# Kernel optimization log

Measured on AMD Instinct MI355X. Metric: run time of the kernel, lower is better.

## Reference

```python
import jax, jax.numpy as jnp
import numpy as np

E, K = 8, 2            # num_experts, top_k
H, DFF = 1024, 2048    # embd_dim, d_ff
B, S = 4, 1024


def setup_inputs() -> dict:
    key = jax.random.key(0)
    ks = jax.random.split(key, 5)
    s_in = 1.0 / np.sqrt(H)
    s_ff = 1.0 / np.sqrt(DFF)
    return {
        "x": jax.random.normal(ks[0], (B, S, H), jnp.float32),
        "centroids": jax.random.normal(ks[1], (E, H), jnp.float32),
        # nn.Linear weights are [out, in]
        "gate_w": jax.random.normal(ks[2], (E, DFF, H), jnp.float32) * s_in,
        "up_w": jax.random.normal(ks[3], (E, DFF, H), jnp.float32) * s_in,
        "down_w": jax.random.normal(ks[4], (E, H, DFF), jnp.float32) * s_ff,
        "routing_bias": jnp.zeros((E,), jnp.float32),
    }


def reference(x, centroids, gate_w, up_w, down_w, routing_bias):
    Bb, Ss, Hh = x.shape
    xf = x.reshape(-1, Hh)  # [T, H]
    # sigmoid affinity router + (non-trainable) routing bias
    affinity = jax.nn.sigmoid(xf @ centroids.T)          # [T, E]
    topk_scores, topk_idx = jax.lax.top_k(affinity + routing_bias, K)  # [T, K]
    topk_w = jax.nn.softmax(topk_scores, axis=-1)        # [T, K]

    # Dense per-expert SwiGLU FFN on all tokens (same math as the
    # sort/gather grouped loop; selection happens in the gather below).
    g = jnp.einsum('th,efh->etf', xf, gate_w)            # [E, T, DFF]
    u = jnp.einsum('th,efh->etf', xf, up_w)              # [E, T, DFF]
    y = jnp.einsum('etf,ehf->eth', jax.nn.silu(g) * u, down_w)  # [E, T, H]

    yt = jnp.transpose(y, (1, 0, 2))                     # [T, E, H]
    sel = jnp.take_along_axis(yt, topk_idx[:, :, None], axis=1)  # [T, K, H]
    out_flat = jnp.sum(sel * topk_w[:, :, None], axis=1)  # [T, H]

    counts = jnp.bincount(topk_idx.ravel(), length=E)    # per-expert token counts
    return out_flat.reshape(Bb, Ss, Hh), counts
```

## Files before the change

kernel.cpp:

```cpp
#include <hip/hip_runtime.h>
#include <math.h>

constexpr int E = 8, H = 1024, DFF = 2048, T = 4096;
constexpr int TR = 8192;
constexpr int MAXJ = 72;

typedef __bf16 bf16x8 __attribute__((ext_vector_type(8)));
typedef __bf16 bf16x4 __attribute__((ext_vector_type(4)));
typedef float f32x4 __attribute__((ext_vector_type(4)));

__device__ __forceinline__ void gload16(const void* g, void* l) {
    __builtin_amdgcn_global_load_lds(
        (const __attribute__((address_space(1))) unsigned int*)g,
        (__attribute__((address_space(3))) unsigned int*)l, 16, 0, 0);
}

__global__ __launch_bounds__(256) void k0_fused(
    const float* __restrict__ x, const float* __restrict__ cent,
    const float* __restrict__ bias,
    int* __restrict__ se, float* __restrict__ sw,
    const float* __restrict__ gw, __bf16* __restrict__ gwb,
    const float* __restrict__ uw, __bf16* __restrict__ uwb,
    __bf16* __restrict__ xb, int w4, int x4) {
    __shared__ float cs[E * H];
    int tid = threadIdx.x;

    if (blockIdx.x >= 1024) {
        int i = (blockIdx.x - 1024) * 256 + tid;
        const float* in; __bf16* out; int idx;
        if (i < w4) { in = gw; out = gwb; idx = i; }
        else if (i < 2 * w4) { in = uw; out = uwb; idx = i - w4; }
        else { idx = i - 2 * w4; if (idx >= x4) return; in = x; out = xb; }
        float4 v = ((const float4*)in)[idx];
        bf16x4 o = {(__bf16)v.x, (__bf16)v.y, (__bf16)v.z, (__bf16)v.w};
        ((bf16x4*)out)[idx] = o;
        return;
    }

    for (int i = tid; i < E * H / 4; i += 256)
        ((float4*)cs)[i] = ((const float4*)cent)[i];
    __syncthreads();

    int wave = tid >> 6, lane = tid & 63;
    int t = blockIdx.x * 4 + wave;
    const float4* xr = (const float4*)(x + (size_t)t * H);
    float acc[E] = {};
    #pragma unroll
    for (int it = 0; it < 4; it++) {
        float4 xv = xr[lane + it * 64];
        #pragma unroll
        for (int e = 0; e < E; e++) {
            float4 cv = ((const float4*)(cs + e * H))[lane + it * 64];
            acc[e] = fmaf(xv.x, cv.x, acc[e]);
            acc[e] = fmaf(xv.y, cv.y, acc[e]);
            acc[e] = fmaf(xv.z, cv.z, acc[e]);
            acc[e] = fmaf(xv.w, cv.w, acc[e]);
        }
    }
    #pragma unroll
    for (int off = 32; off; off >>= 1)
        #pragma unroll
        for (int e = 0; e < E; e++) acc[e] += __shfl_down(acc[e], off);

    if (lane == 0) {
        float s[E];
        #pragma unroll
        for (int e = 0; e < E; e++)
            s[e] = 1.0f / (1.0f + expf(-acc[e])) + bias[e];
        int i0 = 0;
        for (int e = 1; e < E; e++) if (s[e] > s[i0]) i0 = e;
        int i1 = -1;
        for (int e = 0; e < E; e++) {
            if (e == i0) continue;
            if (i1 < 0 || s[e] > s[i1]) i1 = e;
        }
        float m = fmaxf(s[i0], s[i1]);
        float w0 = expf(s[i0] - m), w1 = expf(s[i1] - m);
        float inv = 1.0f / (w0 + w1);
        se[2 * t] = i0;     sw[2 * t] = w0 * inv;
        se[2 * t + 1] = i1; sw[2 * t + 1] = w1 * inv;
    }
}

__global__ __launch_bounds__(1024) void k1b_partition(
    const int* __restrict__ se, int* __restrict__ token_list,
    int* __restrict__ sp, int* __restrict__ cnt) {
    int e = blockIdx.x;
    int tid = threadIdx.x;
    int wave = tid >> 6, lane = tid & 63;
    __shared__ int wsum[16];
    int running = 0;
    for (int c0 = 0; c0 < 2 * T; c0 += 1024) {
        int i = c0 + tid;
        bool pred = (se[i] == e);
        unsigned long long mask = __ballot(pred);
        int pos_in_wave = __popcll(mask & ((1ull << lane) - 1ull));
        if (lane == 0) wsum[wave] = __popcll(mask);
        __syncthreads();
        int wbase = 0;
        #pragma unroll
        for (int w2 = 0; w2 < 16; w2++) {
            int v = wsum[w2];
            if (w2 < wave) wbase += v;
        }
        int total = 0;
        #pragma unroll
        for (int w2 = 0; w2 < 16; w2++) total += wsum[w2];
        if (pred) {
            int p = running + wbase + pos_in_wave;
            token_list[e * T + p] = i >> 1;
            sp[i] = p;
        }
        running += total;
        __syncthreads();
    }
    if (tid == 0) cnt[e] = running;
}

__global__ void k15_offsets(const int* __restrict__ cnt, int* __restrict__ off,
                            float* __restrict__ out_counts,
                            int* __restrict__ jobs, int* __restrict__ njobs) {
    if (threadIdx.x == 0) {
        int acc = 0, nj = 0;
        for (int e = 0; e < E; e++) {
            off[e] = acc; acc += cnt[e];
            int mts = (cnt[e] + 127) >> 7;
            for (int mt = 0; mt < mts; mt++) jobs[nj++] = e * 64 + mt;
        }
        njobs[0] = nj;
    }
    if (threadIdx.x < E) out_counts[threadIdx.x] = (float)cnt[threadIdx.x];
}

__global__ __launch_bounds__(256) void k_conv(const float* __restrict__ in,
                                              __bf16* __restrict__ out, int n4) {
    int i = blockIdx.x * 256 + threadIdx.x;
    if (i < n4) {
        float4 v = ((const float4*)in)[i];
        bf16x4 o = {(__bf16)v.x, (__bf16)v.y, (__bf16)v.z, (__bf16)v.w};
        ((bf16x4*)out)[i] = o;
    }
}

__global__ __launch_bounds__(256, 2) void k2_gateup(
    const __bf16* __restrict__ xb, const __bf16* __restrict__ gwb,
    const __bf16* __restrict__ uwb, const int* __restrict__ cnt,
    const int* __restrict__ off, const int* __restrict__ token_list,
    const int* __restrict__ jobs, const int* __restrict__ njobs,
    __bf16* __restrict__ h) {
    int jt = blockIdx.x >> 4, nt = blockIdx.x & 15;
    if (jt >= njobs[0]) return;
    int job = jobs[jt];
    int e = job >> 6, mt = job & 63;
    int Me = cnt[e], offe = off[e];

    __shared__ __bf16 As[128 * 64];
    __shared__ __bf16 Bg[128 * 64];
    __shared__ __bf16 Bu[128 * 64];

    int tid = threadIdx.x;
    int lane = tid & 63, w = tid >> 6;
    int wm = w >> 1, wn = w & 1;

    const __bf16* asrc[4];
    const __bf16 *bsg[4], *bsu[4];
    #pragma unroll
    for (int rr = 0; rr < 4; rr++) {
        int l = rr * 256 + tid;
        int row = l >> 3, sl = l & 7;
        int gr = mt * 128 + row; if (gr >= Me) gr = Me - 1;
        int tok = token_list[e * T + gr];
        asrc[rr] = xb + (size_t)tok * H + ((sl ^ (row & 7)) * 8);
        size_t base = ((size_t)e * DFF + nt * 128 + row) * H + ((sl ^ (row & 7)) * 8);
        bsg[rr] = gwb + base;
        bsu[rr] = uwb + base;
    }

    f32x4 accg[4][4] = {};
    f32x4 accu[4][4] = {};
    int kq = lane >> 4, m15 = lane & 15;

    for (int k0 = 0; k0 < H; k0 += 64) {
        #pragma unroll
        for (int rr = 0; rr < 4; rr++) {
            gload16(asrc[rr] + k0, &As[(rr * 256 + tid) * 8]);
            gload16(bsg[rr] + k0, &Bg[(rr * 256 + tid) * 8]);
            gload16(bsu[rr] + k0, &Bu[(rr * 256 + tid) * 8]);
        }
        __syncthreads();

        #pragma unroll
        for (int kc = 0; kc < 2; kc++) {
            bf16x8 af[4], gf[4], uf[4];
            #pragma unroll
            for (int i = 0; i < 4; i++) {
                int row = wm * 64 + i * 16 + m15;
                int sl = (kc * 4 + kq) ^ (row & 7);
                af[i] = *(const bf16x8*)&As[row * 64 + sl * 8];
            }
            #pragma unroll
            for (int j = 0; j < 4; j++) {
                int row = wn * 64 + j * 16 + m15;
                int sl = (kc * 4 + kq) ^ (row & 7);
                gf[j] = *(const bf16x8*)&Bg[row * 64 + sl * 8];
                uf[j] = *(const bf16x8*)&Bu[row * 64 + sl * 8];
            }
            #pragma unroll
            for (int i = 0; i < 4; i++)
                #pragma unroll
                for (int j = 0; j < 4; j++) {
                    accg[i][j] = __builtin_amdgcn_mfma_f32_16x16x32_bf16(af[i], gf[j], accg[i][j], 0, 0, 0);
                    accu[i][j] = __builtin_amdgcn_mfma_f32_16x16x32_bf16(af[i], uf[j], accu[i][j], 0, 0, 0);
                }
        }
        __syncthreads();
    }

    #pragma unroll
    for (int i = 0; i < 4; i++)
        #pragma unroll
        for (int j = 0; j < 4; j++) {
            int nloc = wn * 64 + j * 16 + m15;
            size_t c = (size_t)nt * 128 + nloc;
            #pragma unroll
            for (int p = 0; p < 4; p++) {
                int mloc = wm * 64 + i * 16 + kq * 4 + p;
                int mrow = mt * 128 + mloc;
                if (mrow < Me) {
                    float g = accg[i][j][p], u = accu[i][j][p];
                    float sig = 1.0f / (1.0f + __expf(-g));
                    h[(size_t)(offe + mrow) * DFF + c] = (__bf16)(g * sig * u);
                }
            }
        }
}

__global__ __launch_bounds__(256, 2) void k3_down(
    const __bf16* __restrict__ h, const __bf16* __restrict__ dwb,
    const int* __restrict__ cnt, const int* __restrict__ off,
    const int* __restrict__ jobs, const int* __restrict__ njobs,
    __bf16* __restrict__ y) {
    int jt = blockIdx.x >> 3, nt = blockIdx.x & 7;
    if (jt >= njobs[0]) return;
    int job = jobs[jt];
    int e = job >> 6, mt = job & 63;
    int Me = cnt[e], offe = off[e];

    __shared__ __bf16 As[128 * 64];
    __shared__ __bf16 Bs[128 * 64];

    int tid = threadIdx.x;
    int lane = tid & 63, w = tid >> 6;
    int wm = w >> 1, wn = w & 1;

    const __bf16* asrc[4];
    const __bf16* bsrc[4];
    #pragma unroll
    for (int rr = 0; rr < 4; rr++) {
        int l = rr * 256 + tid;
        int row = l >> 3, sl = l & 7;
        int koff = (sl ^ (row & 7)) * 8;
        int gr = mt * 128 + row; if (gr >= Me) gr = Me - 1;
        asrc[rr] = h + (size_t)(offe + gr) * DFF + koff;
        bsrc[rr] = dwb + ((size_t)e * H + nt * 128 + row) * DFF + koff;
    }

    f32x4 acc[4][4] = {};
    int kq = lane >> 4, m15 = lane & 15;

    for (int k0 = 0; k0 < DFF; k0 += 64) {
        #pragma unroll
        for (int rr = 0; rr < 4; rr++)
            gload16(asrc[rr] + k0, &As[(rr * 256 + tid) * 8]);
        #pragma unroll
        for (int rr = 0; rr < 4; rr++)
            gload16(bsrc[rr] + k0, &Bs[(rr * 256 + tid) * 8]);
        __syncthreads();

        #pragma unroll
        for (int kc = 0; kc < 2; kc++) {
            bf16x8 af[4], bf[4];
            #pragma unroll
            for (int i = 0; i < 4; i++) {
                int row = wm * 64 + i * 16 + m15;
                int sl = (kc * 4 + kq) ^ (row & 7);
                af[i] = *(const bf16x8*)&As[row * 64 + sl * 8];
            }
            #pragma unroll
            for (int j = 0; j < 4; j++) {
                int row = wn * 64 + j * 16 + m15;
                int sl = (kc * 4 + kq) ^ (row & 7);
                bf[j] = *(const bf16x8*)&Bs[row * 64 + sl * 8];
            }
            #pragma unroll
            for (int i = 0; i < 4; i++)
                #pragma unroll
                for (int j = 0; j < 4; j++)
                    acc[i][j] = __builtin_amdgcn_mfma_f32_16x16x32_bf16(af[i], bf[j], acc[i][j], 0, 0, 0);
        }
        __syncthreads();
    }

    #pragma unroll
    for (int i = 0; i < 4; i++)
        #pragma unroll
        for (int j = 0; j < 4; j++) {
            int nglob = nt * 128 + wn * 64 + j * 16 + m15;
            #pragma unroll
            for (int p = 0; p < 4; p++) {
                int mloc = wm * 64 + i * 16 + kq * 4 + p;
                int mrow = mt * 128 + mloc;
                if (mrow < Me)
                    y[(size_t)(offe + mrow) * H + nglob] = (__bf16)acc[i][j][p];
            }
        }
}

__global__ __launch_bounds__(256) void k_gather(
    const __bf16* __restrict__ y, const int* __restrict__ se,
    const int* __restrict__ sp, const float* __restrict__ sw,
    const int* __restrict__ off, float* __restrict__ out) {
    int t = blockIdx.x;
    int r0 = off[se[2 * t]] + sp[2 * t];
    int r1 = off[se[2 * t + 1]] + sp[2 * t + 1];
    float w0 = sw[2 * t], w1 = sw[2 * t + 1];
    const bf16x4* y0 = (const bf16x4*)(y + (size_t)r0 * H);
    const bf16x4* y1 = (const bf16x4*)(y + (size_t)r1 * H);
    float4* o = (float4*)(out + (size_t)t * H);
    int c = threadIdx.x;
    bf16x4 a = y0[c], b = y1[c];
    float4 v;
    v.x = w0 * (float)a[0] + w1 * (float)b[0];
    v.y = w0 * (float)a[1] + w1 * (float)b[1];
    v.z = w0 * (float)a[2] + w1 * (float)b[2];
    v.w = w0 * (float)a[3] + w1 * (float)b[3];
    o[c] = v;
}

extern "C" void kernel_launch(void* const* d_in, const int* in_sizes, int n_in,
                              void* d_out, int out_size, void* d_ws, size_t ws_size,
                              hipStream_t stream) {
    const float* x    = (const float*)d_in[0];
    const float* cent = (const float*)d_in[1];
    const float* gw   = (const float*)d_in[2];
    const float* uw   = (const float*)d_in[3];
    const float* dw   = (const float*)d_in[4];
    const float* bias = (const float*)d_in[5];
    float* out = (float*)d_out;

    char* ws = (char*)d_ws;
    int*   cnt        = (int*)(ws + 0);
    int*   off        = (int*)(ws + 64);
    int*   se         = (int*)(ws + 128);
    int*   sp         = (int*)(ws + 128 + 32768);
    float* sw         = (float*)(ws + 128 + 65536);
    int*   token_list = (int*)(ws + 128 + 98304);
    int*   jobs       = (int*)(ws + 229504);
    int*   njobs      = (int*)(ws + 229824);
    const size_t MB = 1u << 20;
    __bf16* gwb = (__bf16*)(ws + 1 * MB);
    __bf16* uwb = (__bf16*)(ws + 1 * MB + 33554432);
    __bf16* dwb = gwb;
    __bf16* y   = uwb;
    __bf16* xb  = (__bf16*)(ws + 1 * MB + 67108864);
    __bf16* h   = (__bf16*)(ws + 1 * MB + 75497472);

    const int W4 = E * DFF * H / 4;
    const int X4 = T * H / 4;
    const int C3 = 2 * W4 + X4;

    k0_fused<<<1024 + (C3 + 255) / 256, 256, 0, stream>>>(
        x, cent, bias, se, sw, gw, gwb, uw, uwb, xb, W4, X4);
    k1b_partition<<<E, 1024, 0, stream>>>(se, token_list, sp, cnt);
    k15_offsets<<<1, 64, 0, stream>>>(cnt, off, out + (size_t)T * H, jobs, njobs);
    k2_gateup<<<MAXJ * 16, 256, 0, stream>>>(xb, gwb, uwb, cnt, off, token_list, jobs, njobs, h);
    k_conv<<<(W4 + 255) / 256, 256, 0, stream>>>(dw, dwb, W4);
    k3_down<<<MAXJ * 8, 256, 0, stream>>>(h, dwb, cnt, off, jobs, njobs, y);
    k_gather<<<T, 256, 0, stream>>>(y, se, sp, sw, off, out);
}
```

Measured before the change: 381.1 us.

## Fuse fp32-to-bf16 weight conversion into the grouped GEMM tile loads

Removes the separate passes that convert the gate, up and down weights to bf16 in workspace. The GEMM kernels now read fp32 weights directly, convert them in registers and store bf16 into LDS, which drops a full write and reread of about 200MB of weight data. In exchange each weight tile is reloaded as fp32 by every M-tile job (up to 72 jobs over 16 or 8 N-tiles), so weight global traffic grows with the number of jobs. The async global-to-LDS path is also replaced by synchronous register loads for B. Launch bounds are raised to 3 blocks per SM.

Result: slower. 598.3 us (+57.0%).

```diff
diff --git a/kernel.cpp b/kernel.cpp
--- a/kernel.cpp
+++ b/kernel.cpp
@@ -19,21 +19,17 @@
     const float* __restrict__ x, const float* __restrict__ cent,
     const float* __restrict__ bias,
     int* __restrict__ se, float* __restrict__ sw,
-    const float* __restrict__ gw, __bf16* __restrict__ gwb,
-    const float* __restrict__ uw, __bf16* __restrict__ uwb,
-    __bf16* __restrict__ xb, int w4, int x4) {
+    __bf16* __restrict__ xb, int x4) {
     __shared__ float cs[E * H];
     int tid = threadIdx.x;
 
     if (blockIdx.x >= 1024) {
         int i = (blockIdx.x - 1024) * 256 + tid;
-        const float* in; __bf16* out; int idx;
-        if (i < w4) { in = gw; out = gwb; idx = i; }
-        else if (i < 2 * w4) { in = uw; out = uwb; idx = i - w4; }
-        else { idx = i - 2 * w4; if (idx >= x4) return; in = x; out = xb; }
-        float4 v = ((const float4*)in)[idx];
-        bf16x4 o = {(__bf16)v.x, (__bf16)v.y, (__bf16)v.z, (__bf16)v.w};
-        ((bf16x4*)out)[idx] = o;
+        if (i < x4) {
+            float4 v = ((const float4*)x)[i];
+            bf16x4 o = {(__bf16)v.x, (__bf16)v.y, (__bf16)v.z, (__bf16)v.w};
+            ((bf16x4*)xb)[i] = o;
+        }
         return;
     }
 
@@ -132,19 +128,9 @@
     if (threadIdx.x < E) out_counts[threadIdx.x] = (float)cnt[threadIdx.x];
 }
 
-__global__ __launch_bounds__(256) void k_conv(const float* __restrict__ in,
-                                              __bf16* __restrict__ out, int n4) {
-    int i = blockIdx.x * 256 + threadIdx.x;
-    if (i < n4) {
-        float4 v = ((const float4*)in)[i];
-        bf16x4 o = {(__bf16)v.x, (__bf16)v.y, (__bf16)v.z, (__bf16)v.w};
-        ((bf16x4*)out)[i] = o;
-    }
-}
-
-__global__ __launch_bounds__(256, 2) void k2_gateup(
-    const __bf16* __restrict__ xb, const __bf16* __restrict__ gwb,
-    const __bf16* __restrict__ uwb, const int* __restrict__ cnt,
+__global__ __launch_bounds__(256, 3) void k2_gateup(
+    const __bf16* __restrict__ xb, const float* __restrict__ gw,
+    const float* __restrict__ uw, const int* __restrict__ cnt,
     const int* __restrict__ off, const int* __restrict__ token_list,
     const int* __restrict__ jobs, const int* __restrict__ njobs,
     __bf16* __restrict__ h) {
@@ -163,17 +149,18 @@
     int wm = w >> 1, wn = w & 1;
 
     const __bf16* asrc[4];
-    const __bf16 *bsg[4], *bsu[4];
+    const float4 *pg[4], *pu[4];
     #pragma unroll
     for (int rr = 0; rr < 4; rr++) {
         int l = rr * 256 + tid;
         int row = l >> 3, sl = l & 7;
+        int ch = sl ^ (row & 7);
         int gr = mt * 128 + row; if (gr >= Me) gr = Me - 1;
         int tok = token_list[e * T + gr];
-        asrc[rr] = xb + (size_t)tok * H + ((sl ^ (row & 7)) * 8);
-        size_t base = ((size_t)e * DFF + nt * 128 + row) * H + ((sl ^ (row & 7)) * 8);
-        bsg[rr] = gwb + base;
-        bsu[rr] = uwb + base;
+        asrc[rr] = xb + (size_t)tok * H + ch * 8;
+        size_t fbase = ((size_t)e * DFF + nt * 128 + row) * H + ch * 8;
+        pg[rr] = (const float4*)(gw + fbase);
+        pu[rr] = (const float4*)(uw + fbase);
     }
 
     f32x4 accg[4][4] = {};
@@ -181,11 +168,20 @@
     int kq = lane >> 4, m15 = lane & 15;
 
     for (int k0 = 0; k0 < H; k0 += 64) {
+        int k4 = k0 >> 2;
+        #pragma unroll
+        for (int rr = 0; rr < 4; rr++)
+            gload16(asrc[rr] + k0, &As[(rr * 256 + tid) * 8]);
         #pragma unroll
         for (int rr = 0; rr < 4; rr++) {
-            gload16(asrc[rr] + k0, &As[(rr * 256 + tid) * 8]);
-            gload16(bsg[rr] + k0, &Bg[(rr * 256 + tid) * 8]);
-            gload16(bsu[rr] + k0, &Bu[(rr * 256 + tid) * 8]);
+            float4 g0 = pg[rr][k4], g1 = pg[rr][k4 + 1];
+            float4 u0 = pu[rr][k4], u1 = pu[rr][k4 + 1];
+            bf16x8 gv = {(__bf16)g0.x, (__bf16)g0.y, (__bf16)g0.z, (__bf16)g0.w,
+                         (__bf16)g1.x, (__bf16)g1.y, (__bf16)g1.z, (__bf16)g1.w};
+            bf16x8 uv = {(__bf16)u0.x, (__bf16)u0.y, (__bf16)u0.z, (__bf16)u0.w,
+                         (__bf16)u1.x, (__bf16)u1.y, (__bf16)u1.z, (__bf16)u1.w};
+            *(bf16x8*)&Bg[(rr * 256 + tid) * 8] = gv;
+            *(bf16x8*)&Bu[(rr * 256 + tid) * 8] = uv;
         }
         __syncthreads();
 
@@ -235,8 +231,8 @@
         }
 }
 
-__global__ __launch_bounds__(256, 2) void k3_down(
-    const __bf16* __restrict__ h, const __bf16* __restrict__ dwb,
+__global__ __launch_bounds__(256, 3) void k3_down(
+    const __bf16* __restrict__ h, const float* __restrict__ dw,
     const int* __restrict__ cnt, const int* __restrict__ off,
     const int* __restrict__ jobs, const int* __restrict__ njobs,
     __bf16* __restrict__ y) {
@@ -254,32 +250,37 @@
     int wm = w >> 1, wn = w & 1;
 
     const __bf16* asrc[4];
-    const __bf16* bsrc[4];
+    const float4* pb[4];
     #pragma unroll
     for (int rr = 0; rr < 4; rr++) {
         int l = rr * 256 + tid;
         int row = l >> 3, sl = l & 7;
-        int koff = (sl ^ (row & 7)) * 8;
+        int ch = sl ^ (row & 7);
         int gr = mt * 128 + row; if (gr >= Me) gr = Me - 1;
-        asrc[rr] = h + (size_t)(offe + gr) * DFF + koff;
-        bsrc[rr] = dwb + ((size_t)e * H + nt * 128 + row) * DFF + koff;
+        asrc[rr] = h + (size_t)(offe + gr) * DFF + ch * 8;
+        pb[rr] = (const float4*)(dw + ((size_t)e * H + nt * 128 + row) * DFF + ch * 8);
     }
 
     f32x4 acc[4][4] = {};
     int kq = lane >> 4, m15 = lane & 15;
 
     for (int k0 = 0; k0 < DFF; k0 += 64) {
+        int k4 = k0 >> 2;
         #pragma unroll
         for (int rr = 0; rr < 4; rr++)
             gload16(asrc[rr] + k0, &As[(rr * 256 + tid) * 8]);
         #pragma unroll
-        for (int rr = 0; rr < 4; rr++)
-            gload16(bsrc[rr] + k0, &Bs[(rr * 256 + tid) * 8]);
+        for (int rr = 0; rr < 4; rr++) {
+            float4 b0 = pb[rr][k4], b1 = pb[rr][k4 + 1];
+            bf16x8 bv = {(__bf16)b0.x, (__bf16)b0.y, (__bf16)b0.z, (__bf16)b0.w,
+                         (__bf16)b1.x, (__bf16)b1.y, (__bf16)b1.z, (__bf16)b1.w};
+            *(bf16x8*)&Bs[(rr * 256 + tid) * 8] = bv;
+        }
         __syncthreads();
 
         #pragma unroll
         for (int kc = 0; kc < 2; kc++) {
-            bf16x8 af[4], bf[4];
+            bf16x8 af[4], bfr[4];
             #pragma unroll
             for (int i = 0; i < 4; i++) {
                 int row = wm * 64 + i * 16 + m15;
@@ -290,13 +291,13 @@
             for (int j = 0; j < 4; j++) {
                 int row = wn * 64 + j * 16 + m15;
                 int sl = (kc * 4 + kq) ^ (row & 7);
-                bf[j] = *(const bf16x8*)&Bs[row * 64 + sl * 8];
+                bfr[j] = *(const bf16x8*)&Bs[row * 64 + sl * 8];
             }
             #pragma unroll
             for (int i = 0; i < 4; i++)
                 #pragma unroll
                 for (int j = 0; j < 4; j++)
-                    acc[i][j] = __builtin_amdgcn_mfma_f32_16x16x32_bf16(af[i], bf[j], acc[i][j], 0, 0, 0);
+                    acc[i][j] = __builtin_amdgcn_mfma_f32_16x16x32_bf16(af[i], bfr[j], acc[i][j], 0, 0, 0);
         }
         __syncthreads();
     }
@@ -358,23 +359,17 @@
     int*   jobs       = (int*)(ws + 229504);
     int*   njobs      = (int*)(ws + 229824);
     const size_t MB = 1u << 20;
-    __bf16* gwb = (__bf16*)(ws + 1 * MB);
-    __bf16* uwb = (__bf16*)(ws + 1 * MB + 33554432);
-    __bf16* dwb = gwb;
-    __bf16* y   = uwb;
-    __bf16* xb  = (__bf16*)(ws + 1 * MB + 67108864);
-    __bf16* h   = (__bf16*)(ws + 1 * MB + 75497472);
-
-    const int W4 = E * DFF * H / 4;
+    __bf16* xb = (__bf16*)(ws + 1 * MB);
+    __bf16* h  = (__bf16*)(ws + 1 * MB + 8388608);
+    __bf16* y  = (__bf16*)(ws + 1 * MB + 41943040);
+
     const int X4 = T * H / 4;
-    const int C3 = 2 * W4 + X4;
-
-    k0_fused<<<1024 + (C3 + 255) / 256, 256, 0, stream>>>(
-        x, cent, bias, se, sw, gw, gwb, uw, uwb, xb, W4, X4);
+
+    k0_fused<<<1024 + (X4 + 255) / 256, 256, 0, stream>>>(
+        x, cent, bias, se, sw, xb, X4);
     k1b_partition<<<E, 1024, 0, stream>>>(se, token_list, sp, cnt);
     k15_offsets<<<1, 64, 0, stream>>>(cnt, off, out + (size_t)T * H, jobs, njobs);
-    k2_gateup<<<MAXJ * 16, 256, 0, stream>>>(xb, gwb, uwb, cnt, off, token_list, jobs, njobs, h);
-    k_conv<<<(W4 + 255) / 256, 256, 0, stream>>>(dw, dwb, W4);
-    k3_down<<<MAXJ * 8, 256, 0, stream>>>(h, dwb, cnt, off, jobs, njobs, y);
+    k2_gateup<<<MAXJ * 16, 256, 0, stream>>>(xb, gw, uw, cnt, off, token_list, jobs, njobs, h);
+    k3_down<<<MAXJ * 8, 256, 0, stream>>>(h, dw, cnt, off, jobs, njobs, y);
     k_gather<<<T, 256, 0, stream>>>(y, se, sp, sw, off, out);
 }
```
